# Performance work log

Hardware: AMD Instinct MI355X
Metric: run time of the kernel (lower is better)

Reference implementation:

```python
import jax, jax.numpy as jnp
import numpy as np

TH_HIGH = 0.6
TH_LOW = 0.3
NEGPOS_RATIO = 3
VAR0, VAR1 = 0.1, 0.2
IMG_SIZE = 255.0


def point_form(a):
    # (cx,cy,w,h) -> (xmin,ymin,xmax,ymax)
    return jnp.concatenate([a[..., :2] - a[..., 2:] / 2,
                            a[..., :2] + a[..., 2:] / 2], axis=-1)


def jaccard(a, b):
    # a: [B,4] point form, b: [A,4] point form -> IoU [B,A]
    lt = jnp.maximum(a[:, None, :2], b[None, :, :2])
    rb = jnp.minimum(a[:, None, 2:], b[None, :, 2:])
    wh = jnp.clip(rb - lt, 0.0)
    inter = wh[..., 0] * wh[..., 1]
    area_a = ((a[:, 2] - a[:, 0]) * (a[:, 3] - a[:, 1]))[:, None]
    area_b = ((b[:, 2] - b[:, 0]) * (b[:, 3] - b[:, 1]))[None, :]
    return inter / (area_a + area_b - inter)


def encode(matched, priors):
    # matched: point form, priors: center-size form (standard SSD encode)
    g_cxcy = ((matched[..., :2] + matched[..., 2:]) / 2 - priors[..., :2]) / (VAR0 * priors[..., 2:])
    g_wh = jnp.log((matched[..., 2:] - matched[..., :2]) / priors[..., 2:]) / VAR1
    return jnp.concatenate([g_cxcy, g_wh], axis=-1)


def decode(loc, priors):
    # standard SSD decode -> point form boxes
    cxcy = priors[..., :2] + loc[..., :2] * VAR0 * priors[..., 2:]
    wh = priors[..., 2:] * jnp.exp(loc[..., 2:] * VAR1)
    mins = cxcy - wh / 2
    return jnp.concatenate([mins, mins + wh], axis=-1)


def smooth_l1(x):
    ax = jnp.abs(x)
    return jnp.where(ax < 1.0, 0.5 * x * x, ax - 0.5)


def setup_inputs() -> dict:
    key = jax.random.key(0)
    k1, k2, k3, k4 = jax.random.split(key, 4)
    B, G, S = 64, 128, 4
    A = G * G * S  # 65536 anchors
    c = (jnp.arange(G, dtype=jnp.float32) + 0.5) / G
    cxcy = jnp.stack(jnp.meshgrid(c, c, indexing='ij'), axis=-1).reshape(-1, 2)  # [G*G,2]
    scales = jnp.array([0.08, 0.12, 0.2, 0.3], dtype=jnp.float32)
    wh = jnp.stack([scales, scales], axis=-1)  # [S,2]
    anchors = jnp.concatenate([jnp.repeat(cxcy, S, axis=0), jnp.tile(wh, (G * G, 1))], axis=-1)  # [A,4] center-size
    # gt boxes: small jitter around a random anchor so positives exist
    idx = jax.random.randint(k1, (B,), 0, A)
    gt_cs = anchors[idx] * (1.0 + 0.03 * jax.random.normal(k2, (B, 4), dtype=jnp.float32))
    gt_boxes = point_form(gt_cs)  # [B,4] point form
    loc_pred = 0.5 * jax.random.normal(k3, (B, A, 4), dtype=jnp.float32)
    conf_pred = jax.random.normal(k4, (B, A, 2), dtype=jnp.float32)
    return {"loc_pred": loc_pred, "conf_pred": conf_pred, "gt_boxes": gt_boxes, "anchors": anchors}


def reference(loc_pred, conf_pred, gt_boxes, anchors):
    B, A, _ = loc_pred.shape
    pf_anchors = point_form(anchors)
    overlaps = jaccard(gt_boxes, pf_anchors)                      # [B,A]
    labels = (overlaps >= TH_HIGH).astype(jnp.int32) - \
             ((overlaps > TH_LOW) & (overlaps < TH_HIGH)).astype(jnp.int32)
    pos = labels == 1                                             # [B,A]
    neg0 = labels == 0
    N = pos.sum()
    Nf = jnp.maximum(N.astype(loc_pred.dtype), 1.0)

    loc_gt = encode(gt_boxes[:, None, :], anchors[None, :, :])    # [B,A,4]
    elem = smooth_l1(loc_pred - loc_gt)
    loss_loc = (elem * pos[..., None]).sum() / (Nf * 4.0)

    # --- hard negative mining ---
    logp = jax.nn.log_softmax(conf_pred, axis=-1)                 # [B,A,2]
    tgt = pos.astype(jnp.int32)
    nll = -jnp.take_along_axis(logp, tgt[..., None], axis=-1)[..., 0]  # [B,A]
    ce = jnp.where(neg0, nll, 0.0)
    loss_idx = jnp.argsort(-ce, axis=1)                           # descending
    idx_rank = jnp.argsort(loss_idx, axis=1)
    num_pos = pos.sum(axis=1, keepdims=True)
    num_neg = jnp.clip(NEGPOS_RATIO * num_pos, 10, A - 1)
    neg = idx_rank < num_neg                                      # [B,A]

    # --- weighted classification loss over picked pos+neg ---
    sel = pos | neg
    w = jnp.array([1.0 / 3.0, 1.0], dtype=conf_pred.dtype)
    wsel = jnp.where(sel, w[tgt], 0.0)
    loss_cls = (nll * wsel).sum() / wsel.sum()

    # --- accuracies on picked set ---
    pred_cls = jnp.argmax(conf_pred, axis=-1)
    pos_m = sel & (tgt == 1)
    neg_m = sel & (tgt == 0)
    pos_accuracy = ((pred_cls == 1) & pos_m).sum() / jnp.maximum(pos_m.sum(), 1)
    neg_accuracy = ((pred_cls == 0) & neg_m).sum() / jnp.maximum(neg_m.sum(), 1)

    # --- decoded diagnostics (masked means over positives) ---
    decoded = decode(loc_pred, anchors[None, :, :])               # [B,A,4] point form
    pos_err = jnp.linalg.norm((gt_boxes[:, None, :2] - decoded[..., :2]) * IMG_SIZE, axis=-1)
    position_error = (pos_err * pos).sum() / Nf
    size_diff = jnp.abs(gt_boxes[:, None, 2:] - decoded[..., 2:])  # [B,A,2]
    size_errors = (size_diff * pos[..., None]).sum(axis=(0, 1)) / Nf * IMG_SIZE

    return (loss_loc, loss_cls, pos_accuracy, neg_accuracy, position_error, size_errors, N)
```

## Files before the change

kernel.cpp:

```cpp
#include <hip/hip_runtime.h>
#include <math.h>


#define MAXB 64
#define NS 1024
#define NB1 256
#define NB2 4096
#define NB3 2048

struct Accum {
  int row_np[MAXB];
  int row_eq_taken[MAXB];
  float f_loc[NS], f_clsp[NS], f_perr[NS], f_se0[NS], f_se1[NS], f_clsn[NS];
  int i_pcor[NS], i_ncor[NS], i_ntot[NS];
};

__device__ __forceinline__ float iou_f(float4 g, float4 an) {
  float ax0 = an.x - an.z * 0.5f, ay0 = an.y - an.w * 0.5f;
  float ax1 = an.x + an.z * 0.5f, ay1 = an.y + an.w * 0.5f;
  float ltx = fmaxf(g.x, ax0), lty = fmaxf(g.y, ay0);
  float rbx = fminf(g.z, ax1), rby = fminf(g.w, ay1);
  float w = fmaxf(rbx - ltx, 0.f), h = fmaxf(rby - lty, 0.f);
  float inter = w * h;
  float area_g = (g.z - g.x) * (g.w - g.y);
  float area_a = (ax1 - ax0) * (ay1 - ay0);
  return inter / (area_g + area_a - inter);
}

__device__ __forceinline__ float sl1(float x) {
  float ax = fabsf(x);
  return ax < 1.f ? 0.5f * x * x : ax - 0.5f;
}

template <int NB>
__device__ uint2 pick_hist(const unsigned int* __restrict__ h, int kr_in,
                           unsigned int* s_wsum,
                           volatile unsigned int* s_bin,
                           volatile unsigned int* s_kr) {
  int tid = threadIdx.x, lane = tid & 63, wv = tid >> 6;
  constexpr int PER = NB / 256;
  unsigned int loc[PER];
  unsigned int my = 0;
#pragma unroll
  for (int i = 0; i < PER; ++i) {
    loc[i] = h[tid * PER + i];
    my += loc[i];
  }
  unsigned int v = my;
#pragma unroll
  for (int o = 1; o < 64; o <<= 1) {
    unsigned int tv = __shfl_down(v, o, 64);
    if (lane + o < 64) v += tv;
  }
  if (lane == 0) s_wsum[wv] = v;
  __syncthreads();
  unsigned int off = 0;
  for (int w2 = wv + 1; w2 < 4; ++w2) off += s_wsum[w2];
  unsigned int vw = v;
  unsigned int incl = vw + off;
  unsigned int above = incl - my;
  if ((int)above < kr_in && kr_in <= (int)incl) {
    int kk = kr_in - (int)above;
    for (int i = PER - 1; i >= 0; --i) {
      int c = (int)loc[i];
      if (kk <= c) {
        *s_bin = (unsigned int)(tid * PER + i);
        *s_kr = (unsigned int)kk;
        break;
      }
      kk -= c;
    }
  }
  __syncthreads();
  uint2 r;
  r.x = *s_bin;
  r.y = *s_kr;
  __syncthreads();
  return r;
}

__device__ __forceinline__ int row_k(const Accum* acc, int b, int A) {
  int k = 3 * acc->row_np[b];
  if (k < 10) k = 10;
  if (k > A - 1) k = A - 1;
  return k;
}

__global__ __launch_bounds__(256) void k_init(Accum* acc, unsigned int* g1,
                                              unsigned int* g2,
                                              unsigned int* g3) {
  int idx = blockIdx.x * 256 + threadIdx.x;
  int stride = gridDim.x * 256;
  int n0 = (int)(sizeof(Accum) / 4);
  int* p = (int*)acc;
  for (int i = idx; i < n0; i += stride) p[i] = 0;
  for (int i = idx; i < MAXB * NB1; i += stride) g1[i] = 0u;
  for (int i = idx; i < MAXB * NB2; i += stride) g2[i] = 0u;
  for (int i = idx; i < MAXB * NB3; i += stride) g3[i] = 0u;
}

__global__ __launch_bounds__(256) void k_main(
    const float* __restrict__ loc_pred, const float* __restrict__ conf,
    const float* __restrict__ gt, const float* __restrict__ anchors,
    Accum* __restrict__ acc, unsigned int* __restrict__ g1,
    unsigned int* __restrict__ keys, int A) {
  int b = blockIdx.y;
  int tid = threadIdx.x;
  int lane = tid & 63, wv = tid >> 6;
  __shared__ unsigned int hist[4][NB1];
  __shared__ float smf[5][4];
  __shared__ int smi[2][4];
  for (int i = tid; i < 4 * NB1; i += 256) ((unsigned int*)hist)[i] = 0u;
  __syncthreads();

  float4 g4 = reinterpret_cast<const float4*>(gt)[b];
  const float4* conf4 = reinterpret_cast<const float4*>(conf);
  const float4* anc4 = reinterpret_cast<const float4*>(anchors);
  const float4* loc4 = reinterpret_cast<const float4*>(loc_pred);
  int abase = blockIdx.x * 4096;
  long long cbase = ((long long)b * A + abase) >> 1;
  uint2* keys2 = reinterpret_cast<uint2*>(keys);

  float loc_s = 0.f, clsp = 0.f, perr = 0.f, se0 = 0.f, se1 = 0.f;
  int pcnt = 0, pcor = 0;

#pragma unroll
  for (int j = 0; j < 8; ++j) {
    float4 cc = conf4[cbase + tid + j * 256];
    int a0 = abase + 2 * (tid + j * 256);
    uint2 kv;
#pragma unroll
    for (int h = 0; h < 2; ++h) {
      int a = a0 + h;
      float c0 = h ? cc.z : cc.x;
      float c1 = h ? cc.w : cc.y;
      float4 an = anc4[a];
      float ov = iou_f(g4, an);
      unsigned int kk = 0u;
      if (ov <= 0.3f) {
        float m = fmaxf(c0, c1);
        float s = logf(expf(c0 - m) + expf(c1 - m));
        kk = __float_as_uint((m - c0) + s);
      }
      if (c1 > c0) kk |= 0x80000000u;
      if (h) kv.y = kk; else kv.x = kk;
      atomicAdd(&hist[wv][(kk & 0x7FFFFFFFu) >> 23], 1u);
      if (ov >= 0.6f) {
        float4 lp = loc4[(long long)b * A + a];
        float gcx = (g4.x + g4.z) * 0.5f, gcy = (g4.y + g4.w) * 0.5f;
        float gw = g4.z - g4.x, gh = g4.w - g4.y;
        float t0 = (gcx - an.x) / (0.1f * an.z);
        float t1 = (gcy - an.y) / (0.1f * an.w);
        float t2 = logf(gw / an.z) / 0.2f;
        float t3 = logf(gh / an.w) / 0.2f;
        loc_s += sl1(lp.x - t0) + sl1(lp.y - t1) + sl1(lp.z - t2) +
                 sl1(lp.w - t3);
        float m = fmaxf(c0, c1);
        float s = logf(expf(c0 - m) + expf(c1 - m));
        clsp += (m - c1) + s;
        pcnt += 1;
        pcor += (c1 > c0) ? 1 : 0;
        float dcx = an.x + lp.x * 0.1f * an.z;
        float dcy = an.y + lp.y * 0.1f * an.w;
        float dw = an.z * expf(lp.z * 0.2f);
        float dh = an.w * expf(lp.w * 0.2f);
        float dx0 = dcx - dw * 0.5f, dy0 = dcy - dh * 0.5f;
        float ex = (g4.x - dx0) * 255.f, ey = (g4.y - dy0) * 255.f;
        perr += sqrtf(ex * ex + ey * ey);
        se0 += fabsf(g4.z - (dx0 + dw));
        se1 += fabsf(g4.w - (dy0 + dh));
      }
    }
    keys2[cbase + tid + j * 256] = kv;
  }

  __syncthreads();
  for (int i = tid; i < NB1; i += 256) {
    unsigned int h = hist[0][i] + hist[1][i] + hist[2][i] + hist[3][i];
    if (h) atomicAdd(&g1[b * NB1 + i], h);
  }

  float fv[5] = {loc_s, clsp, perr, se0, se1};
  int iv[2] = {pcnt, pcor};
#pragma unroll
  for (int q = 0; q < 5; ++q) {
    float v = fv[q];
#pragma unroll
    for (int o = 32; o > 0; o >>= 1) v += __shfl_down(v, o, 64);
    if (lane == 0) smf[q][wv] = v;
  }
#pragma unroll
  for (int q = 0; q < 2; ++q) {
    int v = iv[q];
#pragma unroll
    for (int o = 32; o > 0; o >>= 1) v += __shfl_down(v, o, 64);
    if (lane == 0) smi[q][wv] = v;
  }
  __syncthreads();
  if (tid == 0) {
    float L = 0, C = 0, P = 0, S0 = 0, S1 = 0;
    int PC = 0, COR = 0;
    for (int w2 = 0; w2 < 4; ++w2) {
      L += smf[0][w2]; C += smf[1][w2]; P += smf[2][w2];
      S0 += smf[3][w2]; S1 += smf[4][w2];
      PC += smi[0][w2]; COR += smi[1][w2];
    }
    if (PC > 0) {
      int slot = (blockIdx.y * gridDim.x + blockIdx.x) & (NS - 1);
      atomicAdd(&acc->row_np[b], PC);
      atomicAdd(&acc->f_loc[slot], L);
      atomicAdd(&acc->f_clsp[slot], C);
      atomicAdd(&acc->f_perr[slot], P);
      atomicAdd(&acc->f_se0[slot], S0);
      atomicAdd(&acc->f_se1[slot], S1);
      atomicAdd(&acc->i_pcor[slot], COR);
    }
  }
}

__device__ __forceinline__ void load_keys16(const unsigned int* __restrict__ keys,
                                            int b, int A, unsigned int* kk) {
  long long base4 = (((long long)b * A) >> 2) + blockIdx.x * 1024 + threadIdx.x;
  const uint4* k4 = reinterpret_cast<const uint4*>(keys);
#pragma unroll
  for (int j = 0; j < 4; ++j) {
    uint4 v = k4[base4 + j * 256];
    kk[4 * j + 0] = v.x; kk[4 * j + 1] = v.y;
    kk[4 * j + 2] = v.z; kk[4 * j + 3] = v.w;
  }
}

__global__ __launch_bounds__(256) void k_h2(const unsigned int* __restrict__ keys,
                                            const unsigned int* __restrict__ g1,
                                            unsigned int* __restrict__ g2,
                                            Accum* __restrict__ acc, int A) {
  int b = blockIdx.y;
  __shared__ unsigned int s_wsum[4];
  __shared__ unsigned int s_bin, s_kr;
  uint2 p1 = pick_hist<NB1>(g1 + b * NB1, row_k(acc, b, A), s_wsum, &s_bin, &s_kr);
  unsigned int kk[16];
  load_keys16(keys, b, A, kk);
#pragma unroll
  for (int j = 0; j < 16; ++j) {
    unsigned int k31 = kk[j] & 0x7FFFFFFFu;
    if ((k31 >> 23) == p1.x)
      atomicAdd(&g2[b * NB2 + ((k31 >> 11) & 0xFFFu)], 1u);
  }
}

__global__ __launch_bounds__(256) void k_h3(const unsigned int* __restrict__ keys,
                                            const unsigned int* __restrict__ g1,
                                            const unsigned int* __restrict__ g2,
                                            unsigned int* __restrict__ g3,
                                            Accum* __restrict__ acc, int A) {
  int b = blockIdx.y;
  __shared__ unsigned int s_wsum[4];
  __shared__ unsigned int s_bin, s_kr;
  uint2 p1 = pick_hist<NB1>(g1 + b * NB1, row_k(acc, b, A), s_wsum, &s_bin, &s_kr);
  uint2 p2 = pick_hist<NB2>(g2 + b * NB2, (int)p1.y, s_wsum, &s_bin, &s_kr);
  unsigned int pref20 = (p1.x << 12) | p2.x;
  unsigned int kk[16];
  load_keys16(keys, b, A, kk);
#pragma unroll
  for (int j = 0; j < 16; ++j) {
    unsigned int k31 = kk[j] & 0x7FFFFFFFu;
    if ((k31 >> 11) == pref20) atomicAdd(&g3[b * NB3 + (k31 & 0x7FFu)], 1u);
  }
}

__global__ __launch_bounds__(256) void k_neg(const unsigned int* __restrict__ keys,
                                             const unsigned int* __restrict__ g1,
                                             const unsigned int* __restrict__ g2,
                                             const unsigned int* __restrict__ g3,
                                             Accum* __restrict__ acc, int A) {
  int b = blockIdx.y;
  int tid = threadIdx.x;
  int lane = tid & 63, wv = tid >> 6;
  __shared__ unsigned int s_wsum[4];
  __shared__ unsigned int s_bin, s_kr;
  __shared__ float smf[4];
  __shared__ int smi[2][4];
  uint2 p1 = pick_hist<NB1>(g1 + b * NB1, row_k(acc, b, A), s_wsum, &s_bin, &s_kr);
  uint2 p2 = pick_hist<NB2>(g2 + b * NB2, (int)p1.y, s_wsum, &s_bin, &s_kr);
  uint2 p3 = pick_hist<NB3>(g3 + b * NB3, (int)p2.y, s_wsum, &s_bin, &s_kr);
  unsigned int thr = (p1.x << 23) | (p2.x << 11) | p3.x;
  int need = (int)p3.y;

  unsigned int kk[16];
  load_keys16(keys, b, A, kk);
  float cls = 0.f;
  int ncnt = 0, ncor = 0;
#pragma unroll
  for (int j = 0; j < 16; ++j) {
    unsigned int k31 = kk[j] & 0x7FFFFFFFu;
    bool s = false;
    if (k31 > thr) {
      s = true;
    } else if (k31 == thr) {
      int ord = atomicAdd(&acc->row_eq_taken[b], 1);
      if (ord < need) s = true;
    }
    if (s) {
      cls += __uint_as_float(k31);
      ncnt += 1;
      ncor += (int)((kk[j] >> 31) ^ 1u);
    }
  }
  {
    float v = cls;
#pragma unroll
    for (int o = 32; o > 0; o >>= 1) v += __shfl_down(v, o, 64);
    if (lane == 0) smf[wv] = v;
  }
  {
    int v = ncnt;
#pragma unroll
    for (int o = 32; o > 0; o >>= 1) v += __shfl_down(v, o, 64);
    if (lane == 0) smi[0][wv] = v;
  }
  {
    int v = ncor;
#pragma unroll
    for (int o = 32; o > 0; o >>= 1) v += __shfl_down(v, o, 64);
    if (lane == 0) smi[1][wv] = v;
  }
  __syncthreads();
  if (tid == 0) {
    float C = smf[0] + smf[1] + smf[2] + smf[3];
    int NC = smi[0][0] + smi[0][1] + smi[0][2] + smi[0][3];
    int COR = smi[1][0] + smi[1][1] + smi[1][2] + smi[1][3];
    if (NC > 0) {
      int slot = (blockIdx.y * gridDim.x + blockIdx.x) & (NS - 1);
      atomicAdd(&acc->f_clsn[slot], C);
      atomicAdd(&acc->i_ntot[slot], NC);
      atomicAdd(&acc->i_ncor[slot], COR);
    }
  }
}

__global__ __launch_bounds__(256) void k_final(const Accum* __restrict__ acc,
                                               float* __restrict__ out, int B) {
  __shared__ float sm[256];
  int t = threadIdx.x;
  float vals[10];
  float s;
  s = 0; for (int i = t; i < NS; i += 256) s += acc->f_loc[i];  vals[0] = s;
  s = 0; for (int i = t; i < NS; i += 256) s += acc->f_clsp[i]; vals[1] = s;
  s = 0; for (int i = t; i < NS; i += 256) s += acc->f_perr[i]; vals[2] = s;
  s = 0; for (int i = t; i < NS; i += 256) s += acc->f_se0[i];  vals[3] = s;
  s = 0; for (int i = t; i < NS; i += 256) s += acc->f_se1[i];  vals[4] = s;
  s = 0; for (int i = t; i < NS; i += 256) s += acc->f_clsn[i]; vals[5] = s;
  s = 0; for (int i = t; i < NS; i += 256) s += (float)acc->i_pcor[i]; vals[6] = s;
  s = 0; for (int i = t; i < NS; i += 256) s += (float)acc->i_ncor[i]; vals[7] = s;
  s = 0; for (int i = t; i < NS; i += 256) s += (float)acc->i_ntot[i]; vals[8] = s;
  s = 0; for (int i = t; i < B;  i += 256) s += (float)acc->row_np[i]; vals[9] = s;
  float tot[10];
  for (int q = 0; q < 10; ++q) {
    sm[t] = vals[q];
    __syncthreads();
    for (int o = 128; o > 0; o >>= 1) {
      if (t < o) sm[t] += sm[t + o];
      __syncthreads();
    }
    tot[q] = sm[0];
    __syncthreads();
  }
  if (t == 0) {
    float N = tot[9];
    float Nf = fmaxf(N, 1.f);
    out[0] = tot[0] / (Nf * 4.f);
    float wsum = N + tot[8] * (1.f / 3.f);
    out[1] = (tot[1] + tot[5] * (1.f / 3.f)) / wsum;
    out[2] = tot[6] / fmaxf(N, 1.f);
    out[3] = tot[7] / fmaxf(tot[8], 1.f);
    out[4] = tot[2] / Nf;
    out[5] = tot[3] / Nf * 255.f;
    out[6] = tot[4] / Nf * 255.f;
    out[7] = N;
  }
}

extern "C" void kernel_launch(void* const* d_in, const int* in_sizes, int n_in,
                              void* d_out, int out_size, void* d_ws,
                              size_t ws_size, hipStream_t stream) {
  (void)n_in; (void)out_size; (void)ws_size;
  const float* loc = (const float*)d_in[0];
  const float* conf = (const float*)d_in[1];
  const float* gt = (const float*)d_in[2];
  const float* anchors = (const float*)d_in[3];
  int B = in_sizes[2] / 4;
  int A = in_sizes[3] / 4;
  float* out = (float*)d_out;

  char* w = (char*)d_ws;
  Accum* acc = (Accum*)w;
  size_t off = (sizeof(Accum) + 255) & ~(size_t)255;
  unsigned int* g1 = (unsigned int*)(w + off);
  off += (size_t)MAXB * NB1 * 4;
  unsigned int* g2 = (unsigned int*)(w + off);
  off += (size_t)MAXB * NB2 * 4;
  unsigned int* g3 = (unsigned int*)(w + off);
  off += (size_t)MAXB * NB3 * 4;
  off = (off + 255) & ~(size_t)255;
  unsigned int* keys = (unsigned int*)(w + off);

  dim3 grid(A / 4096, B);
  k_init<<<128, 256, 0, stream>>>(acc, g1, g2, g3);
  k_main<<<grid, 256, 0, stream>>>(loc, conf, gt, anchors, acc, g1, keys, A);
  k_h2<<<grid, 256, 0, stream>>>(keys, g1, g2, acc, A);
  k_h3<<<grid, 256, 0, stream>>>(keys, g1, g2, g3, acc, A);
  k_neg<<<grid, 256, 0, stream>>>(keys, g1, g2, g3, acc, A);
  k_final<<<1, 256, 0, stream>>>(acc, out, B);
}
```

Baseline: 173.4 us.

## Replace multi-pass radix select with recompute plus candidate compaction and per-slice partials

The top-k threshold search no longer writes a full key buffer and rereads it in three kernels. The second kernel recomputes keys from conf and anchors, builds the level-2 histogram, and compacts only keys at or above the level-1 bin into a per-row candidate buffer. A per-row final kernel then builds the level-3 histogram in shared memory and selects negatives from that small candidate set. It also drops the init kernel by zeroing in-kernel, and replaces atomic accumulators with per-slice partial writes. The risks are recomputing IoU and logsumexp twice, and a row-per-block final kernel with only 64 blocks.

```diff
diff --git a/kernel.cpp b/kernel.cpp
--- a/kernel.cpp
+++ b/kernel.cpp
@@ -3,16 +3,26 @@
 
 
 #define MAXB 64
-#define NS 1024
-#define NB1 256
+#define BPR 16
+#define APB 4096
+#define KPT 16
 #define NB2 4096
 #define NB3 2048
 
 struct Accum {
-  int row_np[MAXB];
-  int row_eq_taken[MAXB];
-  float f_loc[NS], f_clsp[NS], f_perr[NS], f_se0[NS], f_se1[NS], f_clsn[NS];
-  int i_pcor[NS], i_ncor[NS], i_ntot[NS];
+  int pnp[MAXB * BPR];
+  int ppc[MAXB * BPR];
+  float pf_loc[MAXB * BPR];
+  float pf_clsp[MAXB * BPR];
+  float pf_perr[MAXB * BPR];
+  float pf_se0[MAXB * BPR];
+  float pf_se1[MAXB * BPR];
+  int cnum[MAXB];
+  int b1[MAXB];
+  int kr1[MAXB];
+  float row_cls[MAXB];
+  int row_ntot[MAXB];
+  int row_ncor[MAXB];
 };
 
 __device__ __forceinline__ float iou_f(float4 g, float4 an) {
@@ -32,10 +42,40 @@
   return ax < 1.f ? 0.5f * x * x : ax - 0.5f;
 }
 
+__device__ uint2 pick_l1(const unsigned int* __restrict__ g1, int b, int kr_in,
+                         unsigned int* s_ws, volatile unsigned int* s_bin,
+                         volatile unsigned int* s_kr) {
+  int tid = threadIdx.x, lane = tid & 63, wv = tid >> 6;
+  const unsigned int* base = g1 + b * BPR * 256;
+  unsigned int my = 0;
+#pragma unroll
+  for (int s = 0; s < BPR; ++s) my += base[s * 256 + tid];
+  unsigned int v = my;
+#pragma unroll
+  for (int o = 1; o < 64; o <<= 1) {
+    unsigned int t = __shfl_down(v, o, 64);
+    if (lane + o < 64) v += t;
+  }
+  if (lane == 0) s_ws[wv] = v;
+  __syncthreads();
+  unsigned int off = 0;
+  for (int w2 = wv + 1; w2 < 4; ++w2) off += s_ws[w2];
+  unsigned int incl = v + off, above = incl - my;
+  if ((int)above < kr_in && kr_in <= (int)incl) {
+    *s_bin = (unsigned int)tid;
+    *s_kr = (unsigned int)(kr_in - (int)above);
+  }
+  __syncthreads();
+  uint2 r;
+  r.x = *s_bin;
+  r.y = *s_kr;
+  __syncthreads();
+  return r;
+}
+
 template <int NB>
 __device__ uint2 pick_hist(const unsigned int* __restrict__ h, int kr_in,
-                           unsigned int* s_wsum,
-                           volatile unsigned int* s_bin,
+                           unsigned int* s_ws, volatile unsigned int* s_bin,
                            volatile unsigned int* s_kr) {
   int tid = threadIdx.x, lane = tid & 63, wv = tid >> 6;
   constexpr int PER = NB / 256;
@@ -49,18 +89,17 @@
   unsigned int v = my;
 #pragma unroll
   for (int o = 1; o < 64; o <<= 1) {
-    unsigned int tv = __shfl_down(v, o, 64);
-    if (lane + o < 64) v += tv;
-  }
-  if (lane == 0) s_wsum[wv] = v;
+    unsigned int t = __shfl_down(v, o, 64);
+    if (lane + o < 64) v += t;
+  }
+  if (lane == 0) s_ws[wv] = v;
   __syncthreads();
   unsigned int off = 0;
-  for (int w2 = wv + 1; w2 < 4; ++w2) off += s_wsum[w2];
-  unsigned int vw = v;
-  unsigned int incl = vw + off;
-  unsigned int above = incl - my;
+  for (int w2 = wv + 1; w2 < 4; ++w2) off += s_ws[w2];
+  unsigned int incl = v + off, above = incl - my;
   if ((int)above < kr_in && kr_in <= (int)incl) {
     int kk = kr_in - (int)above;
+#pragma unroll
     for (int i = PER - 1; i >= 0; --i) {
       int c = (int)loc[i];
       if (kk <= c) {
@@ -79,47 +118,28 @@
   return r;
 }
 
-__device__ __forceinline__ int row_k(const Accum* acc, int b, int A) {
-  int k = 3 * acc->row_np[b];
-  if (k < 10) k = 10;
-  if (k > A - 1) k = A - 1;
-  return k;
-}
-
-__global__ __launch_bounds__(256) void k_init(Accum* acc, unsigned int* g1,
-                                              unsigned int* g2,
-                                              unsigned int* g3) {
-  int idx = blockIdx.x * 256 + threadIdx.x;
-  int stride = gridDim.x * 256;
-  int n0 = (int)(sizeof(Accum) / 4);
-  int* p = (int*)acc;
-  for (int i = idx; i < n0; i += stride) p[i] = 0;
-  for (int i = idx; i < MAXB * NB1; i += stride) g1[i] = 0u;
-  for (int i = idx; i < MAXB * NB2; i += stride) g2[i] = 0u;
-  for (int i = idx; i < MAXB * NB3; i += stride) g3[i] = 0u;
-}
-
 __global__ __launch_bounds__(256) void k_main(
     const float* __restrict__ loc_pred, const float* __restrict__ conf,
     const float* __restrict__ gt, const float* __restrict__ anchors,
     Accum* __restrict__ acc, unsigned int* __restrict__ g1,
-    unsigned int* __restrict__ keys, int A) {
-  int b = blockIdx.y;
-  int tid = threadIdx.x;
-  int lane = tid & 63, wv = tid >> 6;
-  __shared__ unsigned int hist[4][NB1];
+    unsigned int* __restrict__ g2, int A) {
+  int sl = blockIdx.x, b = blockIdx.y;
+  int linear = b * BPR + sl;
+  int tid = threadIdx.x, lane = tid & 63, wv = tid >> 6;
+  __shared__ unsigned int hist[4][256];
   __shared__ float smf[5][4];
   __shared__ int smi[2][4];
-  for (int i = tid; i < 4 * NB1; i += 256) ((unsigned int*)hist)[i] = 0u;
+  g2[linear * 256 + tid] = 0u;
+  if (linear == 0 && tid < MAXB) acc->cnum[tid] = 0;
+  for (int i = tid; i < 1024; i += 256) ((unsigned int*)hist)[i] = 0u;
   __syncthreads();
 
   float4 g4 = reinterpret_cast<const float4*>(gt)[b];
   const float4* conf4 = reinterpret_cast<const float4*>(conf);
   const float4* anc4 = reinterpret_cast<const float4*>(anchors);
   const float4* loc4 = reinterpret_cast<const float4*>(loc_pred);
-  int abase = blockIdx.x * 4096;
+  int abase = sl * APB;
   long long cbase = ((long long)b * A + abase) >> 1;
-  uint2* keys2 = reinterpret_cast<uint2*>(keys);
 
   float loc_s = 0.f, clsp = 0.f, perr = 0.f, se0 = 0.f, se1 = 0.f;
   int pcnt = 0, pcor = 0;
@@ -128,7 +148,6 @@
   for (int j = 0; j < 8; ++j) {
     float4 cc = conf4[cbase + tid + j * 256];
     int a0 = abase + 2 * (tid + j * 256);
-    uint2 kv;
 #pragma unroll
     for (int h = 0; h < 2; ++h) {
       int a = a0 + h;
@@ -142,9 +161,7 @@
         float s = logf(expf(c0 - m) + expf(c1 - m));
         kk = __float_as_uint((m - c0) + s);
       }
-      if (c1 > c0) kk |= 0x80000000u;
-      if (h) kv.y = kk; else kv.x = kk;
-      atomicAdd(&hist[wv][(kk & 0x7FFFFFFFu) >> 23], 1u);
+      atomicAdd(&hist[wv][kk >> 23], 1u);
       if (ov >= 0.6f) {
         float4 lp = loc4[(long long)b * A + a];
         float gcx = (g4.x + g4.z) * 0.5f, gcy = (g4.y + g4.w) * 0.5f;
@@ -171,14 +188,11 @@
         se1 += fabsf(g4.w - (dy0 + dh));
       }
     }
-    keys2[cbase + tid + j * 256] = kv;
-  }
-
-  __syncthreads();
-  for (int i = tid; i < NB1; i += 256) {
-    unsigned int h = hist[0][i] + hist[1][i] + hist[2][i] + hist[3][i];
-    if (h) atomicAdd(&g1[b * NB1 + i], h);
-  }
+  }
+
+  __syncthreads();
+  g1[linear * 256 + tid] =
+      hist[0][tid] + hist[1][tid] + hist[2][tid] + hist[3][tid];
 
   float fv[5] = {loc_s, clsp, perr, se0, se1};
   int iv[2] = {pcnt, pcor};
@@ -205,105 +219,149 @@
       S0 += smf[3][w2]; S1 += smf[4][w2];
       PC += smi[0][w2]; COR += smi[1][w2];
     }
-    if (PC > 0) {
-      int slot = (blockIdx.y * gridDim.x + blockIdx.x) & (NS - 1);
-      atomicAdd(&acc->row_np[b], PC);
-      atomicAdd(&acc->f_loc[slot], L);
-      atomicAdd(&acc->f_clsp[slot], C);
-      atomicAdd(&acc->f_perr[slot], P);
-      atomicAdd(&acc->f_se0[slot], S0);
-      atomicAdd(&acc->f_se1[slot], S1);
-      atomicAdd(&acc->i_pcor[slot], COR);
-    }
-  }
-}
-
-__device__ __forceinline__ void load_keys16(const unsigned int* __restrict__ keys,
-                                            int b, int A, unsigned int* kk) {
-  long long base4 = (((long long)b * A) >> 2) + blockIdx.x * 1024 + threadIdx.x;
-  const uint4* k4 = reinterpret_cast<const uint4*>(keys);
-#pragma unroll
-  for (int j = 0; j < 4; ++j) {
-    uint4 v = k4[base4 + j * 256];
-    kk[4 * j + 0] = v.x; kk[4 * j + 1] = v.y;
-    kk[4 * j + 2] = v.z; kk[4 * j + 3] = v.w;
-  }
-}
-
-__global__ __launch_bounds__(256) void k_h2(const unsigned int* __restrict__ keys,
-                                            const unsigned int* __restrict__ g1,
-                                            unsigned int* __restrict__ g2,
+    acc->pnp[linear] = PC;
+    acc->ppc[linear] = COR;
+    acc->pf_loc[linear] = L;
+    acc->pf_clsp[linear] = C;
+    acc->pf_perr[linear] = P;
+    acc->pf_se0[linear] = S0;
+    acc->pf_se1[linear] = S1;
+  }
+}
+
+__global__ __launch_bounds__(256) void k_h2c(
+    const float* __restrict__ conf, const float* __restrict__ gt,
+    const float* __restrict__ anchors, Accum* __restrict__ acc,
+    const unsigned int* __restrict__ g1, unsigned int* __restrict__ g2,
+    unsigned int* __restrict__ cbuf, int A) {
+  int sl = blockIdx.x, b = blockIdx.y;
+  int tid = threadIdx.x, lane = tid & 63, wv = tid >> 6;
+  __shared__ unsigned int s_ws[4];
+  __shared__ unsigned int s_bin, s_kr;
+  __shared__ unsigned int h2[NB2];
+  __shared__ unsigned int s_base;
+
+  int np = 0;
+#pragma unroll
+  for (int s = 0; s < BPR; ++s) np += acc->pnp[b * BPR + s];
+  int k = 3 * np;
+  if (k < 10) k = 10;
+  if (k > A - 1) k = A - 1;
+  uint2 p1 = pick_l1(g1, b, k, s_ws, &s_bin, &s_kr);
+  unsigned int bin1 = p1.x;
+  if (sl == 0 && tid == 0) {
+    acc->b1[b] = (int)p1.x;
+    acc->kr1[b] = (int)p1.y;
+  }
+  for (int i = tid; i < NB2; i += 256) h2[i] = 0u;
+  __syncthreads();
+
+  float4 g4 = reinterpret_cast<const float4*>(gt)[b];
+  const float4* conf4 = reinterpret_cast<const float4*>(conf);
+  const float4* anc4 = reinterpret_cast<const float4*>(anchors);
+  int abase = sl * APB;
+  long long cbase = ((long long)b * A + abase) >> 1;
+
+  unsigned int keys[KPT];
+  int cnt = 0;
+#pragma unroll
+  for (int j = 0; j < 8; ++j) {
+    float4 cc = conf4[cbase + tid + j * 256];
+    int a0 = abase + 2 * (tid + j * 256);
+#pragma unroll
+    for (int h = 0; h < 2; ++h) {
+      float c0 = h ? cc.z : cc.x;
+      float c1 = h ? cc.w : cc.y;
+      float4 an = anc4[a0 + h];
+      float ov = iou_f(g4, an);
+      unsigned int kk = 0u;
+      if (ov <= 0.3f) {
+        float m = fmaxf(c0, c1);
+        float s = logf(expf(c0 - m) + expf(c1 - m));
+        kk = __float_as_uint((m - c0) + s);
+      }
+      if (c1 > c0) kk |= 0x80000000u;
+      keys[2 * j + h] = kk;
+      unsigned int top8 = (kk & 0x7FFFFFFFu) >> 23;
+      if (top8 == bin1) atomicAdd(&h2[(kk >> 11) & 0xFFFu], 1u);
+      if (top8 >= bin1) ++cnt;
+    }
+  }
+  __syncthreads();
+  for (int i = tid; i < NB2; i += 256)
+    if (h2[i]) atomicAdd(&g2[b * NB2 + i], h2[i]);
+
+  unsigned int v = (unsigned int)cnt;
+#pragma unroll
+  for (int o = 1; o < 64; o <<= 1) {
+    unsigned int t = __shfl_up(v, o, 64);
+    if (lane >= o) v += t;
+  }
+  if (lane == 63) s_ws[wv] = v;
+  __syncthreads();
+  unsigned int woff = 0;
+  for (int w2 = 0; w2 < wv; ++w2) woff += s_ws[w2];
+  unsigned int excl = woff + v - (unsigned int)cnt;
+  if (tid == 0) {
+    unsigned int total = s_ws[0] + s_ws[1] + s_ws[2] + s_ws[3];
+    s_base = (unsigned int)atomicAdd(&acc->cnum[b], (int)total);
+  }
+  __syncthreads();
+  unsigned int w = s_base + excl;
+  unsigned int* crow = cbuf + (size_t)b * A;
+#pragma unroll
+  for (int j = 0; j < KPT; ++j) {
+    unsigned int kk = keys[j];
+    if (((kk & 0x7FFFFFFFu) >> 23) >= bin1) crow[w++] = kk;
+  }
+}
+
+__global__ __launch_bounds__(256) void k_nf(const unsigned int* __restrict__ g2,
+                                            const unsigned int* __restrict__ cbuf,
                                             Accum* __restrict__ acc, int A) {
-  int b = blockIdx.y;
-  __shared__ unsigned int s_wsum[4];
+  int b = blockIdx.x;
+  int tid = threadIdx.x, lane = tid & 63, wv = tid >> 6;
+  __shared__ unsigned int s_ws[4];
   __shared__ unsigned int s_bin, s_kr;
-  uint2 p1 = pick_hist<NB1>(g1 + b * NB1, row_k(acc, b, A), s_wsum, &s_bin, &s_kr);
-  unsigned int kk[16];
-  load_keys16(keys, b, A, kk);
-#pragma unroll
-  for (int j = 0; j < 16; ++j) {
-    unsigned int k31 = kk[j] & 0x7FFFFFFFu;
-    if ((k31 >> 23) == p1.x)
-      atomicAdd(&g2[b * NB2 + ((k31 >> 11) & 0xFFFu)], 1u);
-  }
-}
-
-__global__ __launch_bounds__(256) void k_h3(const unsigned int* __restrict__ keys,
-                                            const unsigned int* __restrict__ g1,
-                                            const unsigned int* __restrict__ g2,
-                                            unsigned int* __restrict__ g3,
-                                            Accum* __restrict__ acc, int A) {
-  int b = blockIdx.y;
-  __shared__ unsigned int s_wsum[4];
-  __shared__ unsigned int s_bin, s_kr;
-  uint2 p1 = pick_hist<NB1>(g1 + b * NB1, row_k(acc, b, A), s_wsum, &s_bin, &s_kr);
-  uint2 p2 = pick_hist<NB2>(g2 + b * NB2, (int)p1.y, s_wsum, &s_bin, &s_kr);
-  unsigned int pref20 = (p1.x << 12) | p2.x;
-  unsigned int kk[16];
-  load_keys16(keys, b, A, kk);
-#pragma unroll
-  for (int j = 0; j < 16; ++j) {
-    unsigned int k31 = kk[j] & 0x7FFFFFFFu;
-    if ((k31 >> 11) == pref20) atomicAdd(&g3[b * NB3 + (k31 & 0x7FFu)], 1u);
-  }
-}
-
-__global__ __launch_bounds__(256) void k_neg(const unsigned int* __restrict__ keys,
-                                             const unsigned int* __restrict__ g1,
-                                             const unsigned int* __restrict__ g2,
-                                             const unsigned int* __restrict__ g3,
-                                             Accum* __restrict__ acc, int A) {
-  int b = blockIdx.y;
-  int tid = threadIdx.x;
-  int lane = tid & 63, wv = tid >> 6;
-  __shared__ unsigned int s_wsum[4];
-  __shared__ unsigned int s_bin, s_kr;
+  __shared__ unsigned int h3[NB3];
+  __shared__ int s_tie;
   __shared__ float smf[4];
   __shared__ int smi[2][4];
-  uint2 p1 = pick_hist<NB1>(g1 + b * NB1, row_k(acc, b, A), s_wsum, &s_bin, &s_kr);
-  uint2 p2 = pick_hist<NB2>(g2 + b * NB2, (int)p1.y, s_wsum, &s_bin, &s_kr);
-  uint2 p3 = pick_hist<NB3>(g3 + b * NB3, (int)p2.y, s_wsum, &s_bin, &s_kr);
-  unsigned int thr = (p1.x << 23) | (p2.x << 11) | p3.x;
+
+  unsigned int bin1 = (unsigned int)acc->b1[b];
+  int kr1 = acc->kr1[b];
+  uint2 p2 = pick_hist<NB2>(g2 + b * NB2, kr1, s_ws, &s_bin, &s_kr);
+  unsigned int pref20 = (bin1 << 12) | p2.x;
+  int cnt = acc->cnum[b];
+  for (int i = tid; i < NB3; i += 256) h3[i] = 0u;
+  if (tid == 0) s_tie = 0;
+  __syncthreads();
+
+  const unsigned int* crow = cbuf + (size_t)b * A;
+  for (int i = tid; i < cnt; i += 256) {
+    unsigned int k31 = crow[i] & 0x7FFFFFFFu;
+    if ((k31 >> 11) == pref20) atomicAdd(&h3[k31 & 0x7FFu], 1u);
+  }
+  __syncthreads();
+  uint2 p3 = pick_hist<NB3>(h3, (int)p2.y, s_ws, &s_bin, &s_kr);
+  unsigned int thr = (pref20 << 11) | p3.x;
   int need = (int)p3.y;
 
-  unsigned int kk[16];
-  load_keys16(keys, b, A, kk);
   float cls = 0.f;
   int ncnt = 0, ncor = 0;
-#pragma unroll
-  for (int j = 0; j < 16; ++j) {
-    unsigned int k31 = kk[j] & 0x7FFFFFFFu;
+  for (int i = tid; i < cnt; i += 256) {
+    unsigned int kk = crow[i];
+    unsigned int k31 = kk & 0x7FFFFFFFu;
     bool s = false;
     if (k31 > thr) {
       s = true;
     } else if (k31 == thr) {
-      int ord = atomicAdd(&acc->row_eq_taken[b], 1);
-      if (ord < need) s = true;
+      if (atomicAdd(&s_tie, 1) < need) s = true;
     }
     if (s) {
       cls += __uint_as_float(k31);
       ncnt += 1;
-      ncor += (int)((kk[j] >> 31) ^ 1u);
+      ncor += (int)((kk >> 31) ^ 1u);
     }
   }
   {
@@ -326,34 +384,29 @@
   }
   __syncthreads();
   if (tid == 0) {
-    float C = smf[0] + smf[1] + smf[2] + smf[3];
-    int NC = smi[0][0] + smi[0][1] + smi[0][2] + smi[0][3];
-    int COR = smi[1][0] + smi[1][1] + smi[1][2] + smi[1][3];
-    if (NC > 0) {
-      int slot = (blockIdx.y * gridDim.x + blockIdx.x) & (NS - 1);
-      atomicAdd(&acc->f_clsn[slot], C);
-      atomicAdd(&acc->i_ntot[slot], NC);
-      atomicAdd(&acc->i_ncor[slot], COR);
-    }
+    acc->row_cls[b] = smf[0] + smf[1] + smf[2] + smf[3];
+    acc->row_ntot[b] = smi[0][0] + smi[0][1] + smi[0][2] + smi[0][3];
+    acc->row_ncor[b] = smi[1][0] + smi[1][1] + smi[1][2] + smi[1][3];
   }
 }
 
 __global__ __launch_bounds__(256) void k_final(const Accum* __restrict__ acc,
-                                               float* __restrict__ out, int B) {
+                                               float* __restrict__ out) {
   __shared__ float sm[256];
   int t = threadIdx.x;
+  const int NSL = MAXB * BPR;
   float vals[10];
   float s;
-  s = 0; for (int i = t; i < NS; i += 256) s += acc->f_loc[i];  vals[0] = s;
-  s = 0; for (int i = t; i < NS; i += 256) s += acc->f_clsp[i]; vals[1] = s;
-  s = 0; for (int i = t; i < NS; i += 256) s += acc->f_perr[i]; vals[2] = s;
-  s = 0; for (int i = t; i < NS; i += 256) s += acc->f_se0[i];  vals[3] = s;
-  s = 0; for (int i = t; i < NS; i += 256) s += acc->f_se1[i];  vals[4] = s;
-  s = 0; for (int i = t; i < NS; i += 256) s += acc->f_clsn[i]; vals[5] = s;
-  s = 0; for (int i = t; i < NS; i += 256) s += (float)acc->i_pcor[i]; vals[6] = s;
-  s = 0; for (int i = t; i < NS; i += 256) s += (float)acc->i_ncor[i]; vals[7] = s;
-  s = 0; for (int i = t; i < NS; i += 256) s += (float)acc->i_ntot[i]; vals[8] = s;
-  s = 0; for (int i = t; i < B;  i += 256) s += (float)acc->row_np[i]; vals[9] = s;
+  s = 0; for (int i = t; i < NSL; i += 256) s += acc->pf_loc[i];  vals[0] = s;
+  s = 0; for (int i = t; i < NSL; i += 256) s += acc->pf_clsp[i]; vals[1] = s;
+  s = 0; for (int i = t; i < NSL; i += 256) s += acc->pf_perr[i]; vals[2] = s;
+  s = 0; for (int i = t; i < NSL; i += 256) s += acc->pf_se0[i];  vals[3] = s;
+  s = 0; for (int i = t; i < NSL; i += 256) s += acc->pf_se1[i];  vals[4] = s;
+  s = 0; for (int i = t; i < MAXB; i += 256) s += acc->row_cls[i]; vals[5] = s;
+  s = 0; for (int i = t; i < NSL; i += 256) s += (float)acc->ppc[i]; vals[6] = s;
+  s = 0; for (int i = t; i < MAXB; i += 256) s += (float)acc->row_ncor[i]; vals[7] = s;
+  s = 0; for (int i = t; i < MAXB; i += 256) s += (float)acc->row_ntot[i]; vals[8] = s;
+  s = 0; for (int i = t; i < NSL; i += 256) s += (float)acc->pnp[i]; vals[9] = s;
   float tot[10];
   for (int q = 0; q < 10; ++q) {
     sm[t] = vals[q];
@@ -396,19 +449,14 @@
   Accum* acc = (Accum*)w;
   size_t off = (sizeof(Accum) + 255) & ~(size_t)255;
   unsigned int* g1 = (unsigned int*)(w + off);
-  off += (size_t)MAXB * NB1 * 4;
+  off += (size_t)MAXB * BPR * 256 * 4;
   unsigned int* g2 = (unsigned int*)(w + off);
   off += (size_t)MAXB * NB2 * 4;
-  unsigned int* g3 = (unsigned int*)(w + off);
-  off += (size_t)MAXB * NB3 * 4;
-  off = (off + 255) & ~(size_t)255;
-  unsigned int* keys = (unsigned int*)(w + off);
-
-  dim3 grid(A / 4096, B);
-  k_init<<<128, 256, 0, stream>>>(acc, g1, g2, g3);
-  k_main<<<grid, 256, 0, stream>>>(loc, conf, gt, anchors, acc, g1, keys, A);
-  k_h2<<<grid, 256, 0, stream>>>(keys, g1, g2, acc, A);
-  k_h3<<<grid, 256, 0, stream>>>(keys, g1, g2, g3, acc, A);
-  k_neg<<<grid, 256, 0, stream>>>(keys, g1, g2, g3, acc, A);
-  k_final<<<1, 256, 0, stream>>>(acc, out, B);
-}
+  unsigned int* cbuf = (unsigned int*)(w + off);
+
+  dim3 grid(A / APB, B);
+  k_main<<<grid, 256, 0, stream>>>(loc, conf, gt, anchors, acc, g1, g2, A);
+  k_h2c<<<grid, 256, 0, stream>>>(conf, gt, anchors, acc, g1, g2, cbuf, A);
+  k_nf<<<B, 256, 0, stream>>>(g2, cbuf, acc, A);
+  k_final<<<1, 256, 0, stream>>>(acc, out);
+}
```

Result: no change. 174.9 us, median of 2 (+0.9%).
